# Kernel optimization log

Measured on AMD Instinct MI355X. Metric: run time of the kernel, lower is better.

The kernel has to match this reference:

```python
import jax, jax.numpy as jnp
import numpy as np

N_NODES = 10000
N_EDGES = 640000
IN_CH = 128
HID = 256
OUT_CH = 10
NUM_GRAPHS = 64
EPS = 0.0  # non-trainable buffer, initial_eps=0


def setup_inputs() -> dict:
    key = jax.random.key(0)
    ks = jax.random.split(key, 12)
    x = jax.random.normal(ks[0], (N_NODES, IN_CH), dtype=jnp.float32)
    edge_index = jax.random.randint(ks[1], (2, N_EDGES), 0, N_NODES, dtype=jnp.int64)
    batch = jnp.sort(jax.random.randint(ks[2], (N_NODES,), 0, NUM_GRAPHS, dtype=jnp.int64))
    edge_weights = jax.random.uniform(ks[3], (N_EDGES,), dtype=jnp.float32)
    def lin(k, fan_in, fan_out):
        bound = 1.0 / np.sqrt(fan_in)
        kw, kb = jax.random.split(k)
        W = jax.random.uniform(kw, (fan_out, fan_in), minval=-bound, maxval=bound, dtype=jnp.float32)
        b = jax.random.uniform(kb, (fan_out,), minval=-bound, maxval=bound, dtype=jnp.float32)
        return W, b
    W1, b1 = lin(ks[4], IN_CH, HID)
    W2, b2 = lin(ks[5], HID, HID)
    W3, b3 = lin(ks[6], HID, HID)
    Wl, bl = lin(ks[7], HID, OUT_CH)
    return {"x": x, "edge_index": edge_index, "batch": batch, "edge_weights": edge_weights,
            "W1": W1, "b1": b1, "W2": W2, "b2": b2, "W3": W3, "b3": b3, "Wl": Wl, "bl": bl}


def _ginw_conv(x, edge_index, edge_weights, W, b):
    # message: edge_weight * x_j (source nodes), aggregated by add at target i
    src, dst = edge_index[0], edge_index[1]
    msg = edge_weights[:, None] * x[src]           # [E, F]
    agg = jax.ops.segment_sum(msg, dst, num_segments=N_NODES)  # [N, F]
    out = agg + (1.0 + EPS) * x
    return out @ W.T + b


def reference(x, edge_index, batch, edge_weights, W1, b1, W2, b2, W3, b3, Wl, bl):
    h = jax.nn.relu(_ginw_conv(x, edge_index, edge_weights, W1, b1))
    h = jax.nn.relu(_ginw_conv(h, edge_index, edge_weights, W2, b2))
    h = jax.nn.relu(_ginw_conv(h, edge_index, edge_weights, W3, b3))
    # global mean pool over graphs
    sums = jax.ops.segment_sum(h, batch, num_segments=NUM_GRAPHS)        # [G, HID]
    cnts = jax.ops.segment_sum(jnp.ones((N_NODES,), h.dtype), batch, num_segments=NUM_GRAPHS)
    pooled = sums / jnp.maximum(cnts, 1.0)[:, None]
    return pooled @ Wl.T + bl
```

## Files before the change

### kernel.cpp

```cpp
#include <hip/hip_runtime.h>
#include <hip/hip_fp16.h>

namespace {
constexpr int NN   = 10000;
constexpr int NE   = 640000;
constexpr int INC  = 128;
constexpr int HIDC = 256;
constexpr int OUTC = 10;
constexpr int NG   = 64;
constexpr int DCAP = 128;
constexpr int NRG  = 8;
constexpr int RNG  = NN / NRG;
constexpr int SLICES = 32;
constexpr int EPSL   = NE / SLICES;
}

typedef __attribute__((ext_vector_type(8))) _Float16 half8;
typedef __attribute__((ext_vector_type(4))) float f32x4;
typedef __attribute__((ext_vector_type(4))) ushort u16x4;

__device__ __forceinline__ ushort f2h(float f) { return __half_as_ushort(__float2half(f)); }
__device__ __forceinline__ float h2f(ushort u) { return __half2float(__ushort_as_half(u)); }

__global__ __launch_bounds__(256) void zero_kernel(int* __restrict__ deg,
                                                   float* __restrict__ pooled) {
    const int gt = blockIdx.x * 256 + threadIdx.x;
    const int gs = gridDim.x * 256;
    for (int i = gt; i < NN; i += gs) deg[i] = 0;
    for (int i = gt; i < NG * HIDC; i += gs) pooled[i] = 0.0f;
}

__global__ __launch_bounds__(1024) void build_kernel(const int* __restrict__ ei,
                                                     const float* __restrict__ ew,
                                                     int* __restrict__ deg,
                                                     uint* __restrict__ erec,
                                                     const float* __restrict__ x,
                                                     ushort* __restrict__ xh,
                                                     const float* __restrict__ W1,
                                                     ushort* __restrict__ w1h,
                                                     const float* __restrict__ W2,
                                                     ushort* __restrict__ w2h,
                                                     const float* __restrict__ W3,
                                                     ushort* __restrict__ w3h) {
    __shared__ int hist[RNG];
    const int t = threadIdx.x;
    const int rx = blockIdx.x & (NRG - 1);
    const int s  = blockIdx.x >> 3;
    const int nlo = rx * RNG;
    const int ebase = s * EPSL;

    for (int i = t; i < RNG; i += 1024) hist[i] = 0;
    __syncthreads();

    for (int vi = t * 4; vi < EPSL; vi += 4096) {
        const int4 d4 = *(const int4*)(ei + NE + ebase + vi);
        int rl;
        rl = d4.x - nlo; if ((uint)rl < (uint)RNG) atomicAdd(&hist[rl], 1);
        rl = d4.y - nlo; if ((uint)rl < (uint)RNG) atomicAdd(&hist[rl], 1);
        rl = d4.z - nlo; if ((uint)rl < (uint)RNG) atomicAdd(&hist[rl], 1);
        rl = d4.w - nlo; if ((uint)rl < (uint)RNG) atomicAdd(&hist[rl], 1);
    }
    __syncthreads();

    for (int b = t; b < RNG; b += 1024) {
        const int c = hist[b];
        if (c > 0) hist[b] = atomicAdd(&deg[nlo + b], c);
    }
    __syncthreads();

    for (int vi = t * 4; vi < EPSL; vi += 4096) {
        const int4 s4 = *(const int4*)(ei + ebase + vi);
        const int4 d4 = *(const int4*)(ei + NE + ebase + vi);
        const float4 w4 = *(const float4*)(ew + ebase + vi);
        int rl;
        rl = d4.x - nlo;
        if ((uint)rl < (uint)RNG) {
            const int idx = atomicAdd(&hist[rl], 1);
            if (idx < DCAP) erec[((size_t)(nlo + rl) << 7) + idx] = ((uint)s4.x << 16) | f2h(w4.x);
        }
        rl = d4.y - nlo;
        if ((uint)rl < (uint)RNG) {
            const int idx = atomicAdd(&hist[rl], 1);
            if (idx < DCAP) erec[((size_t)(nlo + rl) << 7) + idx] = ((uint)s4.y << 16) | f2h(w4.y);
        }
        rl = d4.z - nlo;
        if ((uint)rl < (uint)RNG) {
            const int idx = atomicAdd(&hist[rl], 1);
            if (idx < DCAP) erec[((size_t)(nlo + rl) << 7) + idx] = ((uint)s4.z << 16) | f2h(w4.z);
        }
        rl = d4.w - nlo;
        if ((uint)rl < (uint)RNG) {
            const int idx = atomicAdd(&hist[rl], 1);
            if (idx < DCAP) erec[((size_t)(nlo + rl) << 7) + idx] = ((uint)s4.w << 16) | f2h(w4.w);
        }
    }

    const int gt = blockIdx.x * 1024 + t;
    const int gs = 256 * 1024;
    {
        const int n4 = NN * INC / 4;
        for (int i = gt; i < n4; i += gs) {
            f32x4 v = __builtin_nontemporal_load((const f32x4*)x + i);
            u16x4 o;
#pragma unroll
            for (int j = 0; j < 4; j++) o[j] = f2h(v[j]);
            __builtin_nontemporal_store(o, (u16x4*)xh + i);
        }
    }
    {
        const int n4 = HIDC * INC / 4;
        for (int i = gt; i < n4; i += gs) {
            f32x4 v = __builtin_nontemporal_load((const f32x4*)W1 + i);
            u16x4 o;
#pragma unroll
            for (int j = 0; j < 4; j++) o[j] = f2h(v[j]);
            __builtin_nontemporal_store(o, (u16x4*)w1h + i);
        }
    }
    {
        const int n4 = HIDC * HIDC / 4;
        for (int i = gt; i < n4; i += gs) {
            f32x4 v = __builtin_nontemporal_load((const f32x4*)W2 + i);
            u16x4 o;
#pragma unroll
            for (int j = 0; j < 4; j++) o[j] = f2h(v[j]);
            __builtin_nontemporal_store(o, (u16x4*)w2h + i);
            f32x4 v3 = __builtin_nontemporal_load((const f32x4*)W3 + i);
            u16x4 o3;
#pragma unroll
            for (int j = 0; j < 4; j++) o3[j] = f2h(v3[j]);
            __builtin_nontemporal_store(o3, (u16x4*)w3h + i);
        }
    }
}

__global__ __launch_bounds__(256) void gather128_kernel(const int* __restrict__ deg,
                                                        const uint* __restrict__ erec,
                                                        const ushort* __restrict__ x,
                                                        ushort* __restrict__ out) {
    constexpr int U = 8;
    const int n = blockIdx.x * 4 + (threadIdx.x >> 6);
    if (n >= NN) return;
    const int lane = threadIdx.x & 63;
    const int sub = lane >> 5;
    const int cl  = lane & 31;
    const int d = min(deg[n], DCAP);
    const int beg = n << 7;
    const size_t loff = (size_t)cl * 4;
    const ushort* xr = x + loff;

    float a0, a1, a2, a3;
    {
        u16x4 v = *(const u16x4*)(x + (size_t)n * INC + loff);
        a0 = sub ? 0.f : h2f(v[0]);
        a1 = sub ? 0.f : h2f(v[1]);
        a2 = sub ? 0.f : h2f(v[2]);
        a3 = sub ? 0.f : h2f(v[3]);
    }

    int e = 0;
    for (; e + 2 * U <= d; e += 2 * U) {
        uint rec[U];
#pragma unroll
        for (int u = 0; u < U; u++) rec[u] = erec[beg + e + 2 * u + sub];
        u16x4 v[U];
#pragma unroll
        for (int u = 0; u < U; u++)
            v[u] = *(const u16x4*)(xr + (size_t)(rec[u] >> 16) * INC);
#pragma unroll
        for (int u = 0; u < U; u++) {
            const float w = h2f((ushort)(rec[u] & 0xFFFFu));
            a0 += w * h2f(v[u][0]);
            a1 += w * h2f(v[u][1]);
            a2 += w * h2f(v[u][2]);
            a3 += w * h2f(v[u][3]);
        }
    }
    for (; e + 2 <= d; e += 2) {
        const uint rec = erec[beg + e + sub];
        const float w = h2f((ushort)(rec & 0xFFFFu));
        const u16x4 v = *(const u16x4*)(xr + (size_t)(rec >> 16) * INC);
        a0 += w * h2f(v[0]); a1 += w * h2f(v[1]); a2 += w * h2f(v[2]); a3 += w * h2f(v[3]);
    }
    if (e < d && sub == 0) {
        const uint rec = erec[beg + e];
        const float w = h2f((ushort)(rec & 0xFFFFu));
        const u16x4 v = *(const u16x4*)(xr + (size_t)(rec >> 16) * INC);
        a0 += w * h2f(v[0]); a1 += w * h2f(v[1]); a2 += w * h2f(v[2]); a3 += w * h2f(v[3]);
    }

    a0 += __shfl_xor(a0, 32, 64);
    a1 += __shfl_xor(a1, 32, 64);
    a2 += __shfl_xor(a2, 32, 64);
    a3 += __shfl_xor(a3, 32, 64);
    if (sub == 0) {
        u16x4 o;
        o[0] = f2h(a0); o[1] = f2h(a1); o[2] = f2h(a2); o[3] = f2h(a3);
        __builtin_nontemporal_store(o, (u16x4*)(out + (size_t)n * INC + loff));
    }
}

__global__ __launch_bounds__(256) void gather_half_kernel(const int* __restrict__ deg,
                                                          const uint* __restrict__ erec,
                                                          const ushort* __restrict__ x,
                                                          ushort* __restrict__ out) {
    constexpr int U = 8;
    const int half = blockIdx.x & 1;
    const int n = (blockIdx.x >> 1) * 4 + (threadIdx.x >> 6);
    if (n >= NN) return;
    const int lane = threadIdx.x & 63;
    const int sub = lane >> 5;
    const int cl  = lane & 31;
    const int d = min(deg[n], DCAP);
    const int beg = n << 7;
    const size_t loff = (size_t)half * 128 + cl * 4;
    const ushort* xr = x + loff;

    float a0, a1, a2, a3;
    {
        u16x4 v = *(const u16x4*)(x + (size_t)n * HIDC + loff);
        a0 = sub ? 0.f : h2f(v[0]);
        a1 = sub ? 0.f : h2f(v[1]);
        a2 = sub ? 0.f : h2f(v[2]);
        a3 = sub ? 0.f : h2f(v[3]);
    }

    int e = 0;
    for (; e + 2 * U <= d; e += 2 * U) {
        uint rec[U];
#pragma unroll
        for (int u = 0; u < U; u++) rec[u] = erec[beg + e + 2 * u + sub];
        u16x4 v[U];
#pragma unroll
        for (int u = 0; u < U; u++)
            v[u] = *(const u16x4*)(xr + (size_t)(rec[u] >> 16) * HIDC);
#pragma unroll
        for (int u = 0; u < U; u++) {
            const float w = h2f((ushort)(rec[u] & 0xFFFFu));
            a0 += w * h2f(v[u][0]);
            a1 += w * h2f(v[u][1]);
            a2 += w * h2f(v[u][2]);
            a3 += w * h2f(v[u][3]);
        }
    }
    for (; e + 2 <= d; e += 2) {
        const uint rec = erec[beg + e + sub];
        const float w = h2f((ushort)(rec & 0xFFFFu));
        const u16x4 v = *(const u16x4*)(xr + (size_t)(rec >> 16) * HIDC);
        a0 += w * h2f(v[0]); a1 += w * h2f(v[1]); a2 += w * h2f(v[2]); a3 += w * h2f(v[3]);
    }
    if (e < d && sub == 0) {
        const uint rec = erec[beg + e];
        const float w = h2f((ushort)(rec & 0xFFFFu));
        const u16x4 v = *(const u16x4*)(xr + (size_t)(rec >> 16) * HIDC);
        a0 += w * h2f(v[0]); a1 += w * h2f(v[1]); a2 += w * h2f(v[2]); a3 += w * h2f(v[3]);
    }

    a0 += __shfl_xor(a0, 32, 64);
    a1 += __shfl_xor(a1, 32, 64);
    a2 += __shfl_xor(a2, 32, 64);
    a3 += __shfl_xor(a3, 32, 64);
    if (sub == 0) {
        u16x4 o;
        o[0] = f2h(a0); o[1] = f2h(a1); o[2] = f2h(a2); o[3] = f2h(a3);
        __builtin_nontemporal_store(o, (u16x4*)(out + (size_t)n * HIDC + loff));
    }
}

template <int K>
__global__ __launch_bounds__(256) void mfma_gemm_kernel(const ushort* __restrict__ A,
                                                        const ushort* __restrict__ Wb,
                                                        const float* __restrict__ bias,
                                                        ushort* __restrict__ C, int M) {
    constexpr int LDW = K + 8;
    __shared__ ushort Ws[64 * LDW];
    const int tid = threadIdx.x;
    const int bm = blockIdx.x * 128;
    const int bn = blockIdx.y * 64;

    constexpr int CPR = K / 8;
    for (int idx = tid; idx < 64 * CPR; idx += 256) {
        int r = idx / CPR, c = idx % CPR;
        uint4 v = *(const uint4*)(Wb + (size_t)(bn + r) * K + c * 8);
        *(uint4*)(&Ws[r * LDW + c * 8]) = v;
    }
    __syncthreads();

    const int wave = tid >> 6;
    const int lane = tid & 63;
    const int lrow = lane & 15;
    const int lq   = lane >> 4;
    const int m0 = bm + wave * 32;

    f32x4 acc[2][4] = {};
    const int r0 = min(m0 + lrow, M - 1);
    const int r1 = min(m0 + 16 + lrow, M - 1);

    for (int k0 = 0; k0 < K; k0 += 32) {
        const int kk = k0 + lq * 8;
        half8 a0 = __builtin_nontemporal_load((const half8*)(A + (size_t)r0 * K + kk));
        half8 a1 = __builtin_nontemporal_load((const half8*)(A + (size_t)r1 * K + kk));
        half8 b[4];
#pragma unroll
        for (int j = 0; j < 4; j++)
            b[j] = *(const half8*)(&Ws[(j * 16 + lrow) * LDW + kk]);
#pragma unroll
        for (int j = 0; j < 4; j++) {
            acc[0][j] = __builtin_amdgcn_mfma_f32_16x16x32_f16(a0, b[j], acc[0][j], 0, 0, 0);
            acc[1][j] = __builtin_amdgcn_mfma_f32_16x16x32_f16(a1, b[j], acc[1][j], 0, 0, 0);
        }
    }

#pragma unroll
    for (int sub = 0; sub < 2; sub++) {
#pragma unroll
        for (int j = 0; j < 4; j++) {
            const int gn = bn + j * 16 + lrow;
            const float bv = bias[gn];
#pragma unroll
            for (int i = 0; i < 4; i++) {
                const int gm = m0 + sub * 16 + lq * 4 + i;
                if (gm < M) {
                    float v = acc[sub][j][i] + bv;
                    v = fmaxf(v, 0.0f);
                    C[(size_t)gm * HIDC + gn] = f2h(v);
                }
            }
        }
    }
}

__global__ __launch_bounds__(256) void mfma_gemm_pool_kernel(const ushort* __restrict__ A,
                                                             const ushort* __restrict__ Wb,
                                                             const float* __restrict__ bias,
                                                             const int* __restrict__ batch,
                                                             float* __restrict__ pooled, int M) {
    constexpr int K = HIDC;
    constexpr int LDW = K + 8;
    __shared__ ushort Ws[64 * LDW];
    __shared__ float pl[6][64];
    const int tid = threadIdx.x;
    const int bm = blockIdx.x * 128;
    const int bn = blockIdx.y * 64;

    constexpr int CPR = K / 8;
    for (int idx = tid; idx < 64 * CPR; idx += 256) {
        int r = idx / CPR, c = idx % CPR;
        uint4 v = *(const uint4*)(Wb + (size_t)(bn + r) * K + c * 8);
        *(uint4*)(&Ws[r * LDW + c * 8]) = v;
    }
    for (int i = tid; i < 6 * 64; i += 256) pl[i >> 6][i & 63] = 0.0f;
    __syncthreads();

    const int wave = tid >> 6;
    const int lane = tid & 63;
    const int lrow = lane & 15;
    const int lq   = lane >> 4;
    const int m0 = bm + wave * 32;
    const int g0 = batch[bm];

    f32x4 acc[2][4] = {};
    const int r0 = min(m0 + lrow, M - 1);
    const int r1 = min(m0 + 16 + lrow, M - 1);

    for (int k0 = 0; k0 < K; k0 += 32) {
        const int kk = k0 + lq * 8;
        half8 a0 = __builtin_nontemporal_load((const half8*)(A + (size_t)r0 * K + kk));
        half8 a1 = __builtin_nontemporal_load((const half8*)(A + (size_t)r1 * K + kk));
        half8 b[4];
#pragma unroll
        for (int j = 0; j < 4; j++)
            b[j] = *(const half8*)(&Ws[(j * 16 + lrow) * LDW + kk]);
#pragma unroll
        for (int j = 0; j < 4; j++) {
            acc[0][j] = __builtin_amdgcn_mfma_f32_16x16x32_f16(a0, b[j], acc[0][j], 0, 0, 0);
            acc[1][j] = __builtin_amdgcn_mfma_f32_16x16x32_f16(a1, b[j], acc[1][j], 0, 0, 0);
        }
    }

#pragma unroll
    for (int sub = 0; sub < 2; sub++) {
#pragma unroll
        for (int i = 0; i < 4; i++) {
            const int gm = m0 + sub * 16 + lq * 4 + i;
            if (gm < M) {
                const int gi = min(batch[gm] - g0, 5);
#pragma unroll
                for (int j = 0; j < 4; j++) {
                    const int gn = bn + j * 16 + lrow;
                    float v = acc[sub][j][i] + bias[gn];
                    v = fmaxf(v, 0.0f);
                    atomicAdd(&pl[gi][j * 16 + lrow], v);
                }
            }
        }
    }
    __syncthreads();

    for (int i = tid; i < 6 * 64; i += 256) {
        const int s = i >> 6, col = i & 63;
        const float v = pl[s][col];
        const int gg = g0 + s;
        if (v != 0.0f && gg < NG)
            atomicAdd(&pooled[(size_t)gg * HIDC + bn + col], v);
    }
}

__device__ __forceinline__ int lower_bound_batch(const int* __restrict__ batch, int val) {
    int lo = 0, hi = NN;
    while (lo < hi) {
        int mid = (lo + hi) >> 1;
        if (batch[mid] < val) lo = mid + 1;
        else hi = mid;
    }
    return lo;
}

__global__ __launch_bounds__(256) void head_kernel(const float* __restrict__ pooled,
                                                   const int* __restrict__ batch,
                                                   const float* __restrict__ Wl,
                                                   const float* __restrict__ bl,
                                                   float* __restrict__ out) {
    __shared__ float s[HIDC];
    __shared__ float s2[OUTC][8];
    const int g = blockIdx.x;
    const int t = threadIdx.x;
    const int lo = lower_bound_batch(batch, g);
    const int hi = lower_bound_batch(batch, g + 1);
    const float inv = 1.0f / fmaxf((float)(hi - lo), 1.0f);
    if (t < HIDC) s[t] = pooled[(size_t)g * HIDC + t] * inv;
    __syncthreads();

    if (t < OUTC * 8) {
        const int oc = t >> 3, q = t & 7;
        float acc = 0.f;
        for (int k = q * 32; k < q * 32 + 32; k++)
            acc += s[k] * Wl[(size_t)oc * HIDC + k];
        s2[oc][q] = acc;
    }
    __syncthreads();
    if (t < OUTC) {
        float acc = bl[t];
#pragma unroll
        for (int q = 0; q < 8; q++) acc += s2[t][q];
        out[(size_t)g * OUTC + t] = acc;
    }
}

extern "C" void kernel_launch(void* const* d_in, const int* in_sizes, int n_in,
                              void* d_out, int out_size, void* d_ws, size_t ws_size,
                              hipStream_t stream) {
    const float* x     = (const float*)d_in[0];
    const int*   ei    = (const int*)d_in[1];
    const int*   batch = (const int*)d_in[2];
    const float* ew    = (const float*)d_in[3];
    const float* W1    = (const float*)d_in[4];
    const float* b1    = (const float*)d_in[5];
    const float* W2    = (const float*)d_in[6];
    const float* b2    = (const float*)d_in[7];
    const float* W3    = (const float*)d_in[8];
    const float* b3    = (const float*)d_in[9];
    const float* Wl    = (const float*)d_in[10];
    const float* bl    = (const float*)d_in[11];

    char* p = (char*)d_ws;
    ushort* xh     = (ushort*)p; p += (size_t)NN * INC * 2;
    ushort* agg128 = (ushort*)p; p += (size_t)NN * INC * 2;
    ushort* agg256 = (ushort*)p; p += (size_t)NN * HIDC * 2;
    ushort* h      = (ushort*)p; p += (size_t)NN * HIDC * 2;
    ushort* w1h    = (ushort*)p; p += (size_t)HIDC * INC * 2;
    ushort* w2h    = (ushort*)p; p += (size_t)HIDC * HIDC * 2;
    ushort* w3h    = (ushort*)p; p += (size_t)HIDC * HIDC * 2;
    uint*   erec   = (uint*)p;   p += (size_t)NN * DCAP * 4;
    int*    deg    = (int*)p;    p += (size_t)NN * 4;
    float*  pooled = (float*)p;  p += (size_t)NG * HIDC * 4;

    zero_kernel<<<32, 256, 0, stream>>>(deg, pooled);
    build_kernel<<<NRG * SLICES, 1024, 0, stream>>>(ei, ew, deg, erec, x, xh,
                                                    W1, w1h, W2, w2h, W3, w3h);

    const int gather_grid = (NN + 3) / 4;
    dim3 gemm_grid((NN + 127) / 128, HIDC / 64);

    gather128_kernel<<<gather_grid, 256, 0, stream>>>(deg, erec, xh, agg128);
    mfma_gemm_kernel<INC><<<gemm_grid, 256, 0, stream>>>(agg128, w1h, b1, h, NN);

    gather_half_kernel<<<gather_grid * 2, 256, 0, stream>>>(deg, erec, h, agg256);
    mfma_gemm_kernel<HIDC><<<gemm_grid, 256, 0, stream>>>(agg256, w2h, b2, h, NN);

    gather_half_kernel<<<gather_grid * 2, 256, 0, stream>>>(deg, erec, h, agg256);
    mfma_gemm_pool_kernel<<<gemm_grid, 256, 0, stream>>>(agg256, w3h, b3, batch, pooled, NN);

    head_kernel<<<NG, 256, 0, stream>>>(pooled, batch, Wl, bl, (float*)d_out);
}
```

Baseline: 241.1 us.

## Fuse gather, GEMM and pooling per layer; fold head into last-block epilogue

Replaces the separate gather and MFMA GEMM kernels with one kernel per layer. Each 16-row block gathers neighbor aggregates into LDS and multiplies them by weights read straight from global memory. The last layer also pools and uses a completion counter so the final block computes the linear head, removing the head kernel. This saves the global round trip of the aggregate buffer and several launches. In exchange, each wave gathers one node at a time with full-row lanes, and every block rereads the weights from global or L2 instead of LDS.

```diff
diff --git a/kernel.cpp b/kernel.cpp
--- a/kernel.cpp
+++ b/kernel.cpp
@@ -13,6 +13,8 @@
 constexpr int RNG  = NN / NRG;
 constexpr int SLICES = 32;
 constexpr int EPSL   = NE / SLICES;
+constexpr int BM   = 16;
+constexpr int NBLK = NN / BM;
 }
 
 typedef __attribute__((ext_vector_type(8))) _Float16 half8;
@@ -23,11 +25,13 @@
 __device__ __forceinline__ float h2f(ushort u) { return __half2float(__ushort_as_half(u)); }
 
 __global__ __launch_bounds__(256) void zero_kernel(int* __restrict__ deg,
-                                                   float* __restrict__ pooled) {
+                                                   float* __restrict__ pooled,
+                                                   int* __restrict__ ctr) {
     const int gt = blockIdx.x * 256 + threadIdx.x;
     const int gs = gridDim.x * 256;
     for (int i = gt; i < NN; i += gs) deg[i] = 0;
     for (int i = gt; i < NG * HIDC; i += gs) pooled[i] = 0.0f;
+    if (gt == 0) *ctr = 0;
 }
 
 __global__ __launch_bounds__(1024) void build_kernel(const int* __restrict__ ei,
@@ -134,278 +138,6 @@
     }
 }
 
-__global__ __launch_bounds__(256) void gather128_kernel(const int* __restrict__ deg,
-                                                        const uint* __restrict__ erec,
-                                                        const ushort* __restrict__ x,
-                                                        ushort* __restrict__ out) {
-    constexpr int U = 8;
-    const int n = blockIdx.x * 4 + (threadIdx.x >> 6);
-    if (n >= NN) return;
-    const int lane = threadIdx.x & 63;
-    const int sub = lane >> 5;
-    const int cl  = lane & 31;
-    const int d = min(deg[n], DCAP);
-    const int beg = n << 7;
-    const size_t loff = (size_t)cl * 4;
-    const ushort* xr = x + loff;
-
-    float a0, a1, a2, a3;
-    {
-        u16x4 v = *(const u16x4*)(x + (size_t)n * INC + loff);
-        a0 = sub ? 0.f : h2f(v[0]);
-        a1 = sub ? 0.f : h2f(v[1]);
-        a2 = sub ? 0.f : h2f(v[2]);
-        a3 = sub ? 0.f : h2f(v[3]);
-    }
-
-    int e = 0;
-    for (; e + 2 * U <= d; e += 2 * U) {
-        uint rec[U];
-#pragma unroll
-        for (int u = 0; u < U; u++) rec[u] = erec[beg + e + 2 * u + sub];
-        u16x4 v[U];
-#pragma unroll
-        for (int u = 0; u < U; u++)
-            v[u] = *(const u16x4*)(xr + (size_t)(rec[u] >> 16) * INC);
-#pragma unroll
-        for (int u = 0; u < U; u++) {
-            const float w = h2f((ushort)(rec[u] & 0xFFFFu));
-            a0 += w * h2f(v[u][0]);
-            a1 += w * h2f(v[u][1]);
-            a2 += w * h2f(v[u][2]);
-            a3 += w * h2f(v[u][3]);
-        }
-    }
-    for (; e + 2 <= d; e += 2) {
-        const uint rec = erec[beg + e + sub];
-        const float w = h2f((ushort)(rec & 0xFFFFu));
-        const u16x4 v = *(const u16x4*)(xr + (size_t)(rec >> 16) * INC);
-        a0 += w * h2f(v[0]); a1 += w * h2f(v[1]); a2 += w * h2f(v[2]); a3 += w * h2f(v[3]);
-    }
-    if (e < d && sub == 0) {
-        const uint rec = erec[beg + e];
-        const float w = h2f((ushort)(rec & 0xFFFFu));
-        const u16x4 v = *(const u16x4*)(xr + (size_t)(rec >> 16) * INC);
-        a0 += w * h2f(v[0]); a1 += w * h2f(v[1]); a2 += w * h2f(v[2]); a3 += w * h2f(v[3]);
-    }
-
-    a0 += __shfl_xor(a0, 32, 64);
-    a1 += __shfl_xor(a1, 32, 64);
-    a2 += __shfl_xor(a2, 32, 64);
-    a3 += __shfl_xor(a3, 32, 64);
-    if (sub == 0) {
-        u16x4 o;
-        o[0] = f2h(a0); o[1] = f2h(a1); o[2] = f2h(a2); o[3] = f2h(a3);
-        __builtin_nontemporal_store(o, (u16x4*)(out + (size_t)n * INC + loff));
-    }
-}
-
-__global__ __launch_bounds__(256) void gather_half_kernel(const int* __restrict__ deg,
-                                                          const uint* __restrict__ erec,
-                                                          const ushort* __restrict__ x,
-                                                          ushort* __restrict__ out) {
-    constexpr int U = 8;
-    const int half = blockIdx.x & 1;
-    const int n = (blockIdx.x >> 1) * 4 + (threadIdx.x >> 6);
-    if (n >= NN) return;
-    const int lane = threadIdx.x & 63;
-    const int sub = lane >> 5;
-    const int cl  = lane & 31;
-    const int d = min(deg[n], DCAP);
-    const int beg = n << 7;
-    const size_t loff = (size_t)half * 128 + cl * 4;
-    const ushort* xr = x + loff;
-
-    float a0, a1, a2, a3;
-    {
-        u16x4 v = *(const u16x4*)(x + (size_t)n * HIDC + loff);
-        a0 = sub ? 0.f : h2f(v[0]);
-        a1 = sub ? 0.f : h2f(v[1]);
-        a2 = sub ? 0.f : h2f(v[2]);
-        a3 = sub ? 0.f : h2f(v[3]);
-    }
-
-    int e = 0;
-    for (; e + 2 * U <= d; e += 2 * U) {
-        uint rec[U];
-#pragma unroll
-        for (int u = 0; u < U; u++) rec[u] = erec[beg + e + 2 * u + sub];
-        u16x4 v[U];
-#pragma unroll
-        for (int u = 0; u < U; u++)
-            v[u] = *(const u16x4*)(xr + (size_t)(rec[u] >> 16) * HIDC);
-#pragma unroll
-        for (int u = 0; u < U; u++) {
-            const float w = h2f((ushort)(rec[u] & 0xFFFFu));
-            a0 += w * h2f(v[u][0]);
-            a1 += w * h2f(v[u][1]);
-            a2 += w * h2f(v[u][2]);
-            a3 += w * h2f(v[u][3]);
-        }
-    }
-    for (; e + 2 <= d; e += 2) {
-        const uint rec = erec[beg + e + sub];
-        const float w = h2f((ushort)(rec & 0xFFFFu));
-        const u16x4 v = *(const u16x4*)(xr + (size_t)(rec >> 16) * HIDC);
-        a0 += w * h2f(v[0]); a1 += w * h2f(v[1]); a2 += w * h2f(v[2]); a3 += w * h2f(v[3]);
-    }
-    if (e < d && sub == 0) {
-        const uint rec = erec[beg + e];
-        const float w = h2f((ushort)(rec & 0xFFFFu));
-        const u16x4 v = *(const u16x4*)(xr + (size_t)(rec >> 16) * HIDC);
-        a0 += w * h2f(v[0]); a1 += w * h2f(v[1]); a2 += w * h2f(v[2]); a3 += w * h2f(v[3]);
-    }
-
-    a0 += __shfl_xor(a0, 32, 64);
-    a1 += __shfl_xor(a1, 32, 64);
-    a2 += __shfl_xor(a2, 32, 64);
-    a3 += __shfl_xor(a3, 32, 64);
-    if (sub == 0) {
-        u16x4 o;
-        o[0] = f2h(a0); o[1] = f2h(a1); o[2] = f2h(a2); o[3] = f2h(a3);
-        __builtin_nontemporal_store(o, (u16x4*)(out + (size_t)n * HIDC + loff));
-    }
-}
-
-template <int K>
-__global__ __launch_bounds__(256) void mfma_gemm_kernel(const ushort* __restrict__ A,
-                                                        const ushort* __restrict__ Wb,
-                                                        const float* __restrict__ bias,
-                                                        ushort* __restrict__ C, int M) {
-    constexpr int LDW = K + 8;
-    __shared__ ushort Ws[64 * LDW];
-    const int tid = threadIdx.x;
-    const int bm = blockIdx.x * 128;
-    const int bn = blockIdx.y * 64;
-
-    constexpr int CPR = K / 8;
-    for (int idx = tid; idx < 64 * CPR; idx += 256) {
-        int r = idx / CPR, c = idx % CPR;
-        uint4 v = *(const uint4*)(Wb + (size_t)(bn + r) * K + c * 8);
-        *(uint4*)(&Ws[r * LDW + c * 8]) = v;
-    }
-    __syncthreads();
-
-    const int wave = tid >> 6;
-    const int lane = tid & 63;
-    const int lrow = lane & 15;
-    const int lq   = lane >> 4;
-    const int m0 = bm + wave * 32;
-
-    f32x4 acc[2][4] = {};
-    const int r0 = min(m0 + lrow, M - 1);
-    const int r1 = min(m0 + 16 + lrow, M - 1);
-
-    for (int k0 = 0; k0 < K; k0 += 32) {
-        const int kk = k0 + lq * 8;
-        half8 a0 = __builtin_nontemporal_load((const half8*)(A + (size_t)r0 * K + kk));
-        half8 a1 = __builtin_nontemporal_load((const half8*)(A + (size_t)r1 * K + kk));
-        half8 b[4];
-#pragma unroll
-        for (int j = 0; j < 4; j++)
-            b[j] = *(const half8*)(&Ws[(j * 16 + lrow) * LDW + kk]);
-#pragma unroll
-        for (int j = 0; j < 4; j++) {
-            acc[0][j] = __builtin_amdgcn_mfma_f32_16x16x32_f16(a0, b[j], acc[0][j], 0, 0, 0);
-            acc[1][j] = __builtin_amdgcn_mfma_f32_16x16x32_f16(a1, b[j], acc[1][j], 0, 0, 0);
-        }
-    }
-
-#pragma unroll
-    for (int sub = 0; sub < 2; sub++) {
-#pragma unroll
-        for (int j = 0; j < 4; j++) {
-            const int gn = bn + j * 16 + lrow;
-            const float bv = bias[gn];
-#pragma unroll
-            for (int i = 0; i < 4; i++) {
-                const int gm = m0 + sub * 16 + lq * 4 + i;
-                if (gm < M) {
-                    float v = acc[sub][j][i] + bv;
-                    v = fmaxf(v, 0.0f);
-                    C[(size_t)gm * HIDC + gn] = f2h(v);
-                }
-            }
-        }
-    }
-}
-
-__global__ __launch_bounds__(256) void mfma_gemm_pool_kernel(const ushort* __restrict__ A,
-                                                             const ushort* __restrict__ Wb,
-                                                             const float* __restrict__ bias,
-                                                             const int* __restrict__ batch,
-                                                             float* __restrict__ pooled, int M) {
-    constexpr int K = HIDC;
-    constexpr int LDW = K + 8;
-    __shared__ ushort Ws[64 * LDW];
-    __shared__ float pl[6][64];
-    const int tid = threadIdx.x;
-    const int bm = blockIdx.x * 128;
-    const int bn = blockIdx.y * 64;
-
-    constexpr int CPR = K / 8;
-    for (int idx = tid; idx < 64 * CPR; idx += 256) {
-        int r = idx / CPR, c = idx % CPR;
-        uint4 v = *(const uint4*)(Wb + (size_t)(bn + r) * K + c * 8);
-        *(uint4*)(&Ws[r * LDW + c * 8]) = v;
-    }
-    for (int i = tid; i < 6 * 64; i += 256) pl[i >> 6][i & 63] = 0.0f;
-    __syncthreads();
-
-    const int wave = tid >> 6;
-    const int lane = tid & 63;
-    const int lrow = lane & 15;
-    const int lq   = lane >> 4;
-    const int m0 = bm + wave * 32;
-    const int g0 = batch[bm];
-
-    f32x4 acc[2][4] = {};
-    const int r0 = min(m0 + lrow, M - 1);
-    const int r1 = min(m0 + 16 + lrow, M - 1);
-
-    for (int k0 = 0; k0 < K; k0 += 32) {
-        const int kk = k0 + lq * 8;
-        half8 a0 = __builtin_nontemporal_load((const half8*)(A + (size_t)r0 * K + kk));
-        half8 a1 = __builtin_nontemporal_load((const half8*)(A + (size_t)r1 * K + kk));
-        half8 b[4];
-#pragma unroll
-        for (int j = 0; j < 4; j++)
-            b[j] = *(const half8*)(&Ws[(j * 16 + lrow) * LDW + kk]);
-#pragma unroll
-        for (int j = 0; j < 4; j++) {
-            acc[0][j] = __builtin_amdgcn_mfma_f32_16x16x32_f16(a0, b[j], acc[0][j], 0, 0, 0);
-            acc[1][j] = __builtin_amdgcn_mfma_f32_16x16x32_f16(a1, b[j], acc[1][j], 0, 0, 0);
-        }
-    }
-
-#pragma unroll
-    for (int sub = 0; sub < 2; sub++) {
-#pragma unroll
-        for (int i = 0; i < 4; i++) {
-            const int gm = m0 + sub * 16 + lq * 4 + i;
-            if (gm < M) {
-                const int gi = min(batch[gm] - g0, 5);
-#pragma unroll
-                for (int j = 0; j < 4; j++) {
-                    const int gn = bn + j * 16 + lrow;
-                    float v = acc[sub][j][i] + bias[gn];
-                    v = fmaxf(v, 0.0f);
-                    atomicAdd(&pl[gi][j * 16 + lrow], v);
-                }
-            }
-        }
-    }
-    __syncthreads();
-
-    for (int i = tid; i < 6 * 64; i += 256) {
-        const int s = i >> 6, col = i & 63;
-        const float v = pl[s][col];
-        const int gg = g0 + s;
-        if (v != 0.0f && gg < NG)
-            atomicAdd(&pooled[(size_t)gg * HIDC + bn + col], v);
-    }
-}
-
 __device__ __forceinline__ int lower_bound_batch(const int* __restrict__ batch, int val) {
     int lo = 0, hi = NN;
     while (lo < hi) {
@@ -416,34 +148,163 @@
     return lo;
 }
 
-__global__ __launch_bounds__(256) void head_kernel(const float* __restrict__ pooled,
-                                                   const int* __restrict__ batch,
-                                                   const float* __restrict__ Wl,
-                                                   const float* __restrict__ bl,
-                                                   float* __restrict__ out) {
-    __shared__ float s[HIDC];
-    __shared__ float s2[OUTC][8];
-    const int g = blockIdx.x;
-    const int t = threadIdx.x;
-    const int lo = lower_bound_batch(batch, g);
-    const int hi = lower_bound_batch(batch, g + 1);
-    const float inv = 1.0f / fmaxf((float)(hi - lo), 1.0f);
-    if (t < HIDC) s[t] = pooled[(size_t)g * HIDC + t] * inv;
+template <int K, int LAYER>
+__global__ __launch_bounds__(256) void fused_layer_kernel(const int* __restrict__ deg,
+                                                          const uint* __restrict__ erec,
+                                                          const ushort* __restrict__ X,
+                                                          const ushort* __restrict__ W,
+                                                          const float* __restrict__ bias,
+                                                          ushort* __restrict__ Y,
+                                                          const int* __restrict__ batch,
+                                                          float* __restrict__ pooled,
+                                                          int* __restrict__ ctr,
+                                                          const float* __restrict__ Wl,
+                                                          const float* __restrict__ bl,
+                                                          float* __restrict__ out) {
+    constexpr int CPL = K / 64;
+    constexpr int U = 8;
+    __shared__ alignas(16) ushort As[BM][K + 8];
+    __shared__ float pl[LAYER == 3 ? 6 : 1][LAYER == 3 ? HIDC : 1];
+
+    const int tid = threadIdx.x;
+    const int wv = tid >> 6, lane = tid & 63;
+    const int bm = blockIdx.x * BM;
+
+    if (LAYER == 3)
+        for (int i = tid; i < 6 * HIDC; i += 256) pl[i >> 8][i & 255] = 0.0f;
+
+    const ushort* xr = X + (size_t)lane * CPL;
+    for (int q = 0; q < 4; q++) {
+        const int n = bm + wv * 4 + q;
+        const int d = min(deg[n], DCAP);
+        const int beg = n << 7;
+
+        float a[CPL];
+        if constexpr (CPL == 4) {
+            u16x4 v = *(const u16x4*)(X + (size_t)n * K + lane * 4);
+#pragma unroll
+            for (int i = 0; i < 4; i++) a[i] = h2f(v[i]);
+        } else {
+            ushort2 v = *(const ushort2*)(X + (size_t)n * K + lane * 2);
+            a[0] = h2f(v.x); a[1] = h2f(v.y);
+        }
+
+        int e = 0;
+        for (; e + U <= d; e += U) {
+            uint rec[U];
+#pragma unroll
+            for (int u = 0; u < U; u++) rec[u] = erec[beg + e + u];
+            ushort v[U][CPL];
+#pragma unroll
+            for (int u = 0; u < U; u++) {
+                if constexpr (CPL == 4)
+                    *(u16x4*)v[u] = *(const u16x4*)(xr + (size_t)(rec[u] >> 16) * K);
+                else
+                    *(ushort2*)v[u] = *(const ushort2*)(xr + (size_t)(rec[u] >> 16) * K);
+            }
+#pragma unroll
+            for (int u = 0; u < U; u++) {
+                const float w = h2f((ushort)(rec[u] & 0xFFFFu));
+#pragma unroll
+                for (int i = 0; i < CPL; i++) a[i] += w * h2f(v[u][i]);
+            }
+        }
+        for (; e < d; e++) {
+            const uint rec = erec[beg + e];
+            const float w = h2f((ushort)(rec & 0xFFFFu));
+            ushort v[CPL];
+            if constexpr (CPL == 4)
+                *(u16x4*)v = *(const u16x4*)(xr + (size_t)(rec >> 16) * K);
+            else
+                *(ushort2*)v = *(const ushort2*)(xr + (size_t)(rec >> 16) * K);
+#pragma unroll
+            for (int i = 0; i < CPL; i++) a[i] += w * h2f(v[i]);
+        }
+
+        ushort o[CPL];
+#pragma unroll
+        for (int i = 0; i < CPL; i++) o[i] = f2h(a[i]);
+        if constexpr (CPL == 4)
+            *(u16x4*)(&As[wv * 4 + q][lane * 4]) = *(u16x4*)o;
+        else
+            *(ushort2*)(&As[wv * 4 + q][lane * 2]) = *(ushort2*)o;
+    }
     __syncthreads();
 
-    if (t < OUTC * 8) {
-        const int oc = t >> 3, q = t & 7;
-        float acc = 0.f;
-        for (int k = q * 32; k < q * 32 + 32; k++)
-            acc += s[k] * Wl[(size_t)oc * HIDC + k];
-        s2[oc][q] = acc;
-    }
-    __syncthreads();
-    if (t < OUTC) {
-        float acc = bl[t];
-#pragma unroll
-        for (int q = 0; q < 8; q++) acc += s2[t][q];
-        out[(size_t)g * OUTC + t] = acc;
+    const int lrow = lane & 15, lq = lane >> 4;
+    const int bn = wv * 64;
+    f32x4 acc[4] = {};
+#pragma unroll
+    for (int k0 = 0; k0 < K; k0 += 32) {
+        const int kk = k0 + lq * 8;
+        half8 av = *(const half8*)(&As[lrow][kk]);
+        half8 b[4];
+#pragma unroll
+        for (int j = 0; j < 4; j++)
+            b[j] = *(const half8*)(W + (size_t)(bn + j * 16 + lrow) * K + kk);
+#pragma unroll
+        for (int j = 0; j < 4; j++)
+            acc[j] = __builtin_amdgcn_mfma_f32_16x16x32_f16(av, b[j], acc[j], 0, 0, 0);
+    }
+
+    if constexpr (LAYER != 3) {
+#pragma unroll
+        for (int j = 0; j < 4; j++) {
+            const int gn = bn + j * 16 + lrow;
+            const float bv = bias[gn];
+#pragma unroll
+            for (int i = 0; i < 4; i++) {
+                const int gm = bm + lq * 4 + i;
+                const float v = fmaxf(acc[j][i] + bv, 0.0f);
+                Y[(size_t)gm * HIDC + gn] = f2h(v);
+            }
+        }
+    } else {
+        const int g0 = batch[bm];
+#pragma unroll
+        for (int i = 0; i < 4; i++) {
+            const int gm = bm + lq * 4 + i;
+            const int gi = min(batch[gm] - g0, 5);
+#pragma unroll
+            for (int j = 0; j < 4; j++) {
+                const int gn = bn + j * 16 + lrow;
+                const float v = fmaxf(acc[j][i] + bias[gn], 0.0f);
+                atomicAdd(&pl[gi][gn], v);
+            }
+        }
+        __syncthreads();
+        for (int i = tid; i < 6 * HIDC; i += 256) {
+            const int s = i >> 8, c = i & 255;
+            const float v = pl[s][c];
+            if (v != 0.0f && g0 + s < NG)
+                atomicAdd(&pooled[(size_t)(g0 + s) * HIDC + c], v);
+        }
+
+        __threadfence();
+        __shared__ int slot;
+        if (tid == 0) slot = atomicAdd(ctr, 1);
+        __syncthreads();
+        if (slot == NBLK - 1) {
+            __shared__ float hp[32][HIDC];
+            for (int gh = 0; gh < 2; gh++) {
+                for (int i = tid; i < 32 * HIDC; i += 256) {
+                    const int g = gh * 32 + (i >> 8);
+                    hp[i >> 8][i & 255] = atomicAdd(&pooled[(size_t)g * HIDC + (i & 255)], 0.0f);
+                }
+                __syncthreads();
+                for (int i = tid; i < 32 * OUTC; i += 256) {
+                    const int g = gh * 32 + i / OUTC, oc = i % OUTC;
+                    const int lo = lower_bound_batch(batch, g);
+                    const int hi = lower_bound_batch(batch, g + 1);
+                    const float inv = 1.0f / fmaxf((float)(hi - lo), 1.0f);
+                    float accv = 0.0f;
+                    for (int k = 0; k < HIDC; k++)
+                        accv += hp[g - gh * 32][k] * Wl[(size_t)oc * HIDC + k];
+                    out[(size_t)g * OUTC + oc] = accv * inv + bl[oc];
+                }
+                __syncthreads();
+            }
+        }
     }
 }
 
@@ -465,31 +326,27 @@
 
     char* p = (char*)d_ws;
     ushort* xh     = (ushort*)p; p += (size_t)NN * INC * 2;
-    ushort* agg128 = (ushort*)p; p += (size_t)NN * INC * 2;
-    ushort* agg256 = (ushort*)p; p += (size_t)NN * HIDC * 2;
-    ushort* h      = (ushort*)p; p += (size_t)NN * HIDC * 2;
+    ushort* h1     = (ushort*)p; p += (size_t)NN * HIDC * 2;
+    ushort* h2     = (ushort*)p; p += (size_t)NN * HIDC * 2;
     ushort* w1h    = (ushort*)p; p += (size_t)HIDC * INC * 2;
     ushort* w2h    = (ushort*)p; p += (size_t)HIDC * HIDC * 2;
     ushort* w3h    = (ushort*)p; p += (size_t)HIDC * HIDC * 2;
     uint*   erec   = (uint*)p;   p += (size_t)NN * DCAP * 4;
     int*    deg    = (int*)p;    p += (size_t)NN * 4;
     float*  pooled = (float*)p;  p += (size_t)NG * HIDC * 4;
-
-    zero_kernel<<<32, 256, 0, stream>>>(deg, pooled);
+    int*    ctr    = (int*)p;    p += 256;
+
+    zero_kernel<<<32, 256, 0, stream>>>(deg, pooled, ctr);
     build_kernel<<<NRG * SLICES, 1024, 0, stream>>>(ei, ew, deg, erec, x, xh,
                                                     W1, w1h, W2, w2h, W3, w3h);
 
-    const int gather_grid = (NN + 3) / 4;
-    dim3 gemm_grid((NN + 127) / 128, HIDC / 64);
-
-    gather128_kernel<<<gather_grid, 256, 0, stream>>>(deg, erec, xh, agg128);
-    mfma_gemm_kernel<INC><<<gemm_grid, 256, 0, stream>>>(agg128, w1h, b1, h, NN);
-
-    gather_half_kernel<<<gather_grid * 2, 256, 0, stream>>>(deg, erec, h, agg256);
-    mfma_gemm_kernel<HIDC><<<gemm_grid, 256, 0, stream>>>(agg256, w2h, b2, h, NN);
-
-    gather_half_kernel<<<gather_grid * 2, 256, 0, stream>>>(deg, erec, h, agg256);
-    mfma_gemm_pool_kernel<<<gemm_grid, 256, 0, stream>>>(agg256, w3h, b3, batch, pooled, NN);
-
-    head_kernel<<<NG, 256, 0, stream>>>(pooled, batch, Wl, bl, (float*)d_out);
-}
+    fused_layer_kernel<INC, 1><<<NBLK, 256, 0, stream>>>(deg, erec, xh, w1h, b1, h1,
+                                                         nullptr, nullptr, nullptr,
+                                                         nullptr, nullptr, nullptr);
+    fused_layer_kernel<HIDC, 2><<<NBLK, 256, 0, stream>>>(deg, erec, h1, w2h, b2, h2,
+                                                          nullptr, nullptr, nullptr,
+                                                          nullptr, nullptr, nullptr);
+    fused_layer_kernel<HIDC, 3><<<NBLK, 256, 0, stream>>>(deg, erec, h2, w3h, b3, h1,
+                                                          batch, pooled, ctr,
+                                                          Wl, bl, (float*)d_out);
+}
```

After: 334.0 us. 38.5% more time.

## Partition gather feature columns by XCC with atomic work queues for L2 locality

Applied to the files above, without the earlier changes.

Replaces the fixed-grid gather kernels with a persistent gather kernel. Feature columns are split into 64-wide quarters (or halves for the 128-wide input), and each block starts on the quarter matching its XCC id, so each chiplet's L2 mostly holds one column slice of the node features. Blocks pull groups of 4 nodes from per-slice atomic counters, which also balances work across blocks. The cost is narrower 4-byte loads per lane, an atomic plus two barriers per group, reliance on a hardware register read through inline asm, and edge records being reread once per column slice.

```diff
diff --git a/kernel.cpp b/kernel.cpp
--- a/kernel.cpp
+++ b/kernel.cpp
@@ -13,6 +13,9 @@
 constexpr int RNG  = NN / NRG;
 constexpr int SLICES = 32;
 constexpr int EPSL   = NE / SLICES;
+constexpr int GRP  = 4;
+constexpr int NGRP = NN / GRP;
+constexpr int GBLK = 2048;
 }
 
 typedef __attribute__((ext_vector_type(8))) _Float16 half8;
@@ -22,12 +25,20 @@
 __device__ __forceinline__ ushort f2h(float f) { return __half_as_ushort(__float2half(f)); }
 __device__ __forceinline__ float h2f(ushort u) { return __half2float(__ushort_as_half(u)); }
 
+__device__ __forceinline__ int get_xcc() {
+    int x;
+    asm volatile("s_getreg_b32 %0, hwreg(HW_REG_XCC_ID)" : "=s"(x));
+    return x & 7;
+}
+
 __global__ __launch_bounds__(256) void zero_kernel(int* __restrict__ deg,
-                                                   float* __restrict__ pooled) {
+                                                   float* __restrict__ pooled,
+                                                   int* __restrict__ qctr) {
     const int gt = blockIdx.x * 256 + threadIdx.x;
     const int gs = gridDim.x * 256;
     for (int i = gt; i < NN; i += gs) deg[i] = 0;
     for (int i = gt; i < NG * HIDC; i += gs) pooled[i] = 0.0f;
+    if (gt < 32) qctr[gt] = 0;
 }
 
 __global__ __launch_bounds__(1024) void build_kernel(const int* __restrict__ ei,
@@ -134,136 +145,81 @@
     }
 }
 
-__global__ __launch_bounds__(256) void gather128_kernel(const int* __restrict__ deg,
-                                                        const uint* __restrict__ erec,
-                                                        const ushort* __restrict__ x,
-                                                        ushort* __restrict__ out) {
+template <int K, int NSPLIT>
+__global__ __launch_bounds__(256) void gatherq_kernel(const int* __restrict__ deg,
+                                                      const uint* __restrict__ erec,
+                                                      const ushort* __restrict__ X,
+                                                      ushort* __restrict__ out,
+                                                      int* __restrict__ qctr) {
     constexpr int U = 8;
-    const int n = blockIdx.x * 4 + (threadIdx.x >> 6);
-    if (n >= NN) return;
-    const int lane = threadIdx.x & 63;
+    __shared__ int sg;
+    const int tid = threadIdx.x;
+    const int wv = tid >> 6, lane = tid & 63;
     const int sub = lane >> 5;
     const int cl  = lane & 31;
-    const int d = min(deg[n], DCAP);
-    const int beg = n << 7;
-    const size_t loff = (size_t)cl * 4;
-    const ushort* xr = x + loff;
-
-    float a0, a1, a2, a3;
-    {
-        u16x4 v = *(const u16x4*)(x + (size_t)n * INC + loff);
-        a0 = sub ? 0.f : h2f(v[0]);
-        a1 = sub ? 0.f : h2f(v[1]);
-        a2 = sub ? 0.f : h2f(v[2]);
-        a3 = sub ? 0.f : h2f(v[3]);
-    }
-
-    int e = 0;
-    for (; e + 2 * U <= d; e += 2 * U) {
-        uint rec[U];
-#pragma unroll
-        for (int u = 0; u < U; u++) rec[u] = erec[beg + e + 2 * u + sub];
-        u16x4 v[U];
-#pragma unroll
-        for (int u = 0; u < U; u++)
-            v[u] = *(const u16x4*)(xr + (size_t)(rec[u] >> 16) * INC);
-#pragma unroll
-        for (int u = 0; u < U; u++) {
-            const float w = h2f((ushort)(rec[u] & 0xFFFFu));
-            a0 += w * h2f(v[u][0]);
-            a1 += w * h2f(v[u][1]);
-            a2 += w * h2f(v[u][2]);
-            a3 += w * h2f(v[u][3]);
-        }
-    }
-    for (; e + 2 <= d; e += 2) {
-        const uint rec = erec[beg + e + sub];
-        const float w = h2f((ushort)(rec & 0xFFFFu));
-        const u16x4 v = *(const u16x4*)(xr + (size_t)(rec >> 16) * INC);
-        a0 += w * h2f(v[0]); a1 += w * h2f(v[1]); a2 += w * h2f(v[2]); a3 += w * h2f(v[3]);
-    }
-    if (e < d && sub == 0) {
-        const uint rec = erec[beg + e];
-        const float w = h2f((ushort)(rec & 0xFFFFu));
-        const u16x4 v = *(const u16x4*)(xr + (size_t)(rec >> 16) * INC);
-        a0 += w * h2f(v[0]); a1 += w * h2f(v[1]); a2 += w * h2f(v[2]); a3 += w * h2f(v[3]);
-    }
-
-    a0 += __shfl_xor(a0, 32, 64);
-    a1 += __shfl_xor(a1, 32, 64);
-    a2 += __shfl_xor(a2, 32, 64);
-    a3 += __shfl_xor(a3, 32, 64);
-    if (sub == 0) {
-        u16x4 o;
-        o[0] = f2h(a0); o[1] = f2h(a1); o[2] = f2h(a2); o[3] = f2h(a3);
-        __builtin_nontemporal_store(o, (u16x4*)(out + (size_t)n * INC + loff));
-    }
-}
-
-__global__ __launch_bounds__(256) void gather_half_kernel(const int* __restrict__ deg,
-                                                          const uint* __restrict__ erec,
-                                                          const ushort* __restrict__ x,
-                                                          ushort* __restrict__ out) {
-    constexpr int U = 8;
-    const int half = blockIdx.x & 1;
-    const int n = (blockIdx.x >> 1) * 4 + (threadIdx.x >> 6);
-    if (n >= NN) return;
-    const int lane = threadIdx.x & 63;
-    const int sub = lane >> 5;
-    const int cl  = lane & 31;
-    const int d = min(deg[n], DCAP);
-    const int beg = n << 7;
-    const size_t loff = (size_t)half * 128 + cl * 4;
-    const ushort* xr = x + loff;
-
-    float a0, a1, a2, a3;
-    {
-        u16x4 v = *(const u16x4*)(x + (size_t)n * HIDC + loff);
-        a0 = sub ? 0.f : h2f(v[0]);
-        a1 = sub ? 0.f : h2f(v[1]);
-        a2 = sub ? 0.f : h2f(v[2]);
-        a3 = sub ? 0.f : h2f(v[3]);
-    }
-
-    int e = 0;
-    for (; e + 2 * U <= d; e += 2 * U) {
-        uint rec[U];
-#pragma unroll
-        for (int u = 0; u < U; u++) rec[u] = erec[beg + e + 2 * u + sub];
-        u16x4 v[U];
-#pragma unroll
-        for (int u = 0; u < U; u++)
-            v[u] = *(const u16x4*)(xr + (size_t)(rec[u] >> 16) * HIDC);
-#pragma unroll
-        for (int u = 0; u < U; u++) {
-            const float w = h2f((ushort)(rec[u] & 0xFFFFu));
-            a0 += w * h2f(v[u][0]);
-            a1 += w * h2f(v[u][1]);
-            a2 += w * h2f(v[u][2]);
-            a3 += w * h2f(v[u][3]);
-        }
-    }
-    for (; e + 2 <= d; e += 2) {
-        const uint rec = erec[beg + e + sub];
-        const float w = h2f((ushort)(rec & 0xFFFFu));
-        const u16x4 v = *(const u16x4*)(xr + (size_t)(rec >> 16) * HIDC);
-        a0 += w * h2f(v[0]); a1 += w * h2f(v[1]); a2 += w * h2f(v[2]); a3 += w * h2f(v[3]);
-    }
-    if (e < d && sub == 0) {
-        const uint rec = erec[beg + e];
-        const float w = h2f((ushort)(rec & 0xFFFFu));
-        const u16x4 v = *(const u16x4*)(xr + (size_t)(rec >> 16) * HIDC);
-        a0 += w * h2f(v[0]); a1 += w * h2f(v[1]); a2 += w * h2f(v[2]); a3 += w * h2f(v[3]);
-    }
-
-    a0 += __shfl_xor(a0, 32, 64);
-    a1 += __shfl_xor(a1, 32, 64);
-    a2 += __shfl_xor(a2, 32, 64);
-    a3 += __shfl_xor(a3, 32, 64);
-    if (sub == 0) {
-        u16x4 o;
-        o[0] = f2h(a0); o[1] = f2h(a1); o[2] = f2h(a2); o[3] = f2h(a3);
-        __builtin_nontemporal_store(o, (u16x4*)(out + (size_t)n * HIDC + loff));
+    const int myq = get_xcc() & (NSPLIT - 1);
+
+    for (int dq = 0; dq < NSPLIT; ++dq) {
+        const int q = (myq + dq) & (NSPLIT - 1);
+        const size_t coff = (size_t)q * 64 + cl * 2;
+        const ushort* xr = X + coff;
+        while (true) {
+            __syncthreads();
+            if (tid == 0) sg = atomicAdd(&qctr[q], 1);
+            __syncthreads();
+            const int g = sg;
+            if (g >= NGRP) break;
+
+            const int n = g * GRP + wv;
+            const int d = min(deg[n], DCAP);
+            const int beg = n << 7;
+
+            float a0, a1;
+            {
+                const uint v = *(const uint*)(X + (size_t)n * K + coff);
+                a0 = sub ? 0.f : h2f((ushort)(v & 0xFFFFu));
+                a1 = sub ? 0.f : h2f((ushort)(v >> 16));
+            }
+
+            int e = 0;
+            for (; e + 2 * U <= d; e += 2 * U) {
+                uint rec[U];
+#pragma unroll
+                for (int u = 0; u < U; u++)
+                    rec[u] = __builtin_nontemporal_load(erec + beg + e + 2 * u + sub);
+                uint v[U];
+#pragma unroll
+                for (int u = 0; u < U; u++)
+                    v[u] = *(const uint*)(xr + (size_t)(rec[u] >> 16) * K);
+#pragma unroll
+                for (int u = 0; u < U; u++) {
+                    const float w = h2f((ushort)(rec[u] & 0xFFFFu));
+                    a0 += w * h2f((ushort)(v[u] & 0xFFFFu));
+                    a1 += w * h2f((ushort)(v[u] >> 16));
+                }
+            }
+            for (; e + 2 <= d; e += 2) {
+                const uint rec = __builtin_nontemporal_load(erec + beg + e + sub);
+                const float w = h2f((ushort)(rec & 0xFFFFu));
+                const uint v = *(const uint*)(xr + (size_t)(rec >> 16) * K);
+                a0 += w * h2f((ushort)(v & 0xFFFFu));
+                a1 += w * h2f((ushort)(v >> 16));
+            }
+            if (e < d && sub == 0) {
+                const uint rec = __builtin_nontemporal_load(erec + beg + e);
+                const float w = h2f((ushort)(rec & 0xFFFFu));
+                const uint v = *(const uint*)(xr + (size_t)(rec >> 16) * K);
+                a0 += w * h2f((ushort)(v & 0xFFFFu));
+                a1 += w * h2f((ushort)(v >> 16));
+            }
+
+            a0 += __shfl_xor(a0, 32, 64);
+            a1 += __shfl_xor(a1, 32, 64);
+            if (sub == 0) {
+                const uint ob = (uint)f2h(a0) | ((uint)f2h(a1) << 16);
+                __builtin_nontemporal_store(ob, (uint*)(out + (size_t)n * K + coff));
+            }
+        }
     }
 }
 
@@ -474,21 +430,21 @@
     uint*   erec   = (uint*)p;   p += (size_t)NN * DCAP * 4;
     int*    deg    = (int*)p;    p += (size_t)NN * 4;
     float*  pooled = (float*)p;  p += (size_t)NG * HIDC * 4;
-
-    zero_kernel<<<32, 256, 0, stream>>>(deg, pooled);
+    int*    qctr   = (int*)p;    p += 128;
+
+    zero_kernel<<<32, 256, 0, stream>>>(deg, pooled, qctr);
     build_kernel<<<NRG * SLICES, 1024, 0, stream>>>(ei, ew, deg, erec, x, xh,
                                                     W1, w1h, W2, w2h, W3, w3h);
 
-    const int gather_grid = (NN + 3) / 4;
     dim3 gemm_grid((NN + 127) / 128, HIDC / 64);
 
-    gather128_kernel<<<gather_grid, 256, 0, stream>>>(deg, erec, xh, agg128);
+    gatherq_kernel<INC, 2><<<GBLK, 256, 0, stream>>>(deg, erec, xh, agg128, qctr + 0);
     mfma_gemm_kernel<INC><<<gemm_grid, 256, 0, stream>>>(agg128, w1h, b1, h, NN);
 
-    gather_half_kernel<<<gather_grid * 2, 256, 0, stream>>>(deg, erec, h, agg256);
+    gatherq_kernel<HIDC, 4><<<GBLK, 256, 0, stream>>>(deg, erec, h, agg256, qctr + 8);
     mfma_gemm_kernel<HIDC><<<gemm_grid, 256, 0, stream>>>(agg256, w2h, b2, h, NN);
 
-    gather_half_kernel<<<gather_grid * 2, 256, 0, stream>>>(deg, erec, h, agg256);
+    gatherq_kernel<HIDC, 4><<<GBLK, 256, 0, stream>>>(deg, erec, h, agg256, qctr + 16);
     mfma_gemm_pool_kernel<<<gemm_grid, 256, 0, stream>>>(agg256, w3h, b3, batch, pooled, NN);
 
     head_kernel<<<NG, 256, 0, stream>>>(pooled, batch, Wl, bl, (float*)d_out);
```

Measured after the change: 703.2 us. 192% more time.
